# Performance work log

Hardware: AMD Instinct MI355X
Metric: run time of the kernel (lower is better)

The kernel has to match this reference:

```python
import jax, jax.numpy as jnp
import numpy as np

N_NODES = 50000

def _gcn_layer(x, src, dst, W, b, n_nodes):
    # x: [N, F_in]; src/dst: [E+N] (self-loops already appended)
    h = x @ W  # [N, F_out]
    deg = jax.ops.segment_sum(jnp.ones_like(dst, dtype=h.dtype), dst, num_segments=n_nodes)
    dinv = jnp.where(deg > 0, jax.lax.rsqrt(deg), 0.0)  # deg^{-1/2}
    norm = dinv[src] * dinv[dst]  # [E+N]
    msg = h[src] * norm[:, None]  # gather + scale
    out = jax.ops.segment_sum(msg, dst, num_segments=n_nodes)  # scatter-add
    return out + b

def setup_inputs() -> dict:
    key = jax.random.key(0)
    k1, k2, k3, k4 = jax.random.split(key, 4)
    d = 128
    E = 800000
    x = jax.random.normal(k1, (N_NODES, d), dtype=jnp.float32)
    edge_index = jax.random.randint(k2, (2, E), 0, N_NODES, dtype=jnp.int64)
    W1 = jax.random.normal(k3, (d, d), dtype=jnp.float32) / np.sqrt(d)
    b1 = jnp.zeros((d,), dtype=jnp.float32)
    W2 = jax.random.normal(k4, (d, d), dtype=jnp.float32) / np.sqrt(d)
    b2 = jnp.zeros((d,), dtype=jnp.float32)
    return {"x": x, "edge_index": edge_index, "W1": W1, "b1": b1, "W2": W2, "b2": b2}

def reference(x, edge_index, W1, b1, W2, b2):
    n = x.shape[0]
    loops = jnp.arange(n, dtype=edge_index.dtype)
    src = jnp.concatenate([edge_index[0], loops])  # add self-loops
    dst = jnp.concatenate([edge_index[1], loops])
    h = _gcn_layer(x, src, dst, W1, b1, n)
    h = jax.nn.relu(h)
    z = _gcn_layer(h, src, dst, W2, b2, n)
    return z
```

## Files before the change

### kernel.cpp

```cpp
#include <hip/hip_runtime.h>
#include <hip/hip_fp16.h>

#define NF 128
#define KC 64
#define NPART 4
#define NPMAX 12544

typedef _Float16 half8 __attribute__((ext_vector_type(8)));
typedef _Float16 half4v __attribute__((ext_vector_type(4)));
typedef float    floatx4 __attribute__((ext_vector_type(4)));

__global__ __launch_bounds__(512) void count2_k(
    const int* __restrict__ dst, unsigned short* __restrict__ pcnt,
    int E, int N, int Ec)
{
    __shared__ int lcnt[NPMAX];
    const int p = blockIdx.x & 3, c = blockIdx.x >> 2;
    const int Np = (N + 3) >> 2;
    const int lo = p * Np, hi = min(lo + Np, N);
    const int sz = hi - lo;
    for (int i = threadIdx.x; i < sz; i += 512) lcnt[i] = 0;
    __syncthreads();

    const int e0 = c * Ec, e1 = min(e0 + Ec, E);
    for (int e = e0 + (int)threadIdx.x * 4; e + 3 < e1; e += 512 * 4) {
        int4 d = *(const int4*)(dst + e);
        if (d.x >= lo && d.x < hi) atomicAdd(&lcnt[d.x - lo], 1);
        if (d.y >= lo && d.y < hi) atomicAdd(&lcnt[d.y - lo], 1);
        if (d.z >= lo && d.z < hi) atomicAdd(&lcnt[d.z - lo], 1);
        if (d.w >= lo && d.w < hi) atomicAdd(&lcnt[d.w - lo], 1);
    }
    int rem0 = e0 + ((e1 - e0) & ~3);
    for (int e = rem0 + (int)threadIdx.x; e < e1; e += 512) {
        int d = dst[e];
        if (d >= lo && d < hi) atomicAdd(&lcnt[d - lo], 1);
    }
    __syncthreads();
    for (int i = threadIdx.x; i < sz; i += 512)
        pcnt[(size_t)c * N + lo + i] = (unsigned short)lcnt[i];
}

__global__ __launch_bounds__(256) void pscan2_k(
    unsigned short* __restrict__ pcnt, float* __restrict__ dinv,
    int* __restrict__ rowptr, int* __restrict__ blocksum, int n, int N, int nb,
    const float* __restrict__ W1, const float* __restrict__ W2,
    __half* __restrict__ WT1, __half* __restrict__ WT2)
{
    if ((int)blockIdx.x >= nb) {
        int idx = ((int)blockIdx.x - nb) * 256 + threadIdx.x;
        const float* W = (idx < 16384) ? W1 : W2;
        __half* WT     = (idx < 16384) ? WT1 : WT2;
        int j = idx & 16383;
        int nn = j & 127, k = j >> 7;
        WT[nn * NF + k] = __float2half(W[k * NF + nn]);
        return;
    }
    __shared__ int sm[256];
    int tid = threadIdx.x;
    int bin = blockIdx.x * 256 + tid;
    int total = 0;
    if (bin < n) {
        #pragma unroll 4
        for (int c = 0; c < KC; c++) {
            size_t o = (size_t)c * N + bin;
            int v = pcnt[o];
            pcnt[o] = (unsigned short)total;
            total += v;
        }
        dinv[bin] = rsqrtf((float)total + 1.0f);
    }
    sm[tid] = total;
    __syncthreads();
    #pragma unroll
    for (int d = 1; d < 256; d <<= 1) {
        int t = (tid >= d) ? sm[tid - d] : 0;
        __syncthreads();
        sm[tid] += t;
        __syncthreads();
    }
    if (bin < n) rowptr[bin] = sm[tid] - total;
    if (tid == 255) blocksum[blockIdx.x] = sm[255];
}


template<bool F32IN>
__device__ __forceinline__ void gemm_body512(
    const void* __restrict__ Xv, const __half* __restrict__ WT,
    const float* __restrict__ dinv, __half* __restrict__ out, int M, int bid,
    __half (*wlds)[136])
{
    const int tid = threadIdx.x;
    {
        int r = tid >> 2;
        int c0 = (tid & 3) * 32;
        const half8* s = (const half8*)(WT + (size_t)r * NF + c0);
        half8* d = (half8*)&wlds[r][c0];
        #pragma unroll
        for (int j = 0; j < 4; j++) d[j] = s[j];
    }
    __syncthreads();

    const int wave = tid >> 6, lane = tid & 63;
    const int quad = lane >> 4, l15 = lane & 15;
    const int rowA = bid * 128 + wave * 16 + l15;
    const int rowc = (rowA < M) ? rowA : (M - 1);

    half8 afr[4];
    if (F32IN) {
        const float* X = (const float*)Xv;
        #pragma unroll
        for (int kc = 0; kc < 4; kc++) {
            const floatx4* p = (const floatx4*)(X + (size_t)rowc * NF + kc * 32 + quad * 8);
            floatx4 u = p[0], v = p[1];
            half8 a;
            a[0] = (_Float16)u[0]; a[1] = (_Float16)u[1];
            a[2] = (_Float16)u[2]; a[3] = (_Float16)u[3];
            a[4] = (_Float16)v[0]; a[5] = (_Float16)v[1];
            a[6] = (_Float16)v[2]; a[7] = (_Float16)v[3];
            afr[kc] = a;
        }
    } else {
        const __half* X = (const __half*)Xv;
        #pragma unroll
        for (int kc = 0; kc < 4; kc++)
            afr[kc] = *(const half8*)(X + (size_t)rowc * NF + kc * 32 + quad * 8);
    }

    floatx4 acc[8];
    #pragma unroll
    for (int ct = 0; ct < 8; ct++) { floatx4 z = {0.f, 0.f, 0.f, 0.f}; acc[ct] = z; }

    #pragma unroll
    for (int kc = 0; kc < 4; kc++) {
        #pragma unroll
        for (int ct = 0; ct < 8; ct++) {
            half8 b = *(const half8*)&wlds[ct * 16 + l15][kc * 32 + quad * 8];
            acc[ct] = __builtin_amdgcn_mfma_f32_16x16x32_f16(afr[kc], b, acc[ct], 0, 0, 0);
        }
    }

    const int orow0 = bid * 128 + wave * 16 + quad * 4;
    #pragma unroll
    for (int r = 0; r < 4; r++) {
        int orow = orow0 + r;
        if (orow < M) {
            float s = dinv[orow];
            #pragma unroll
            for (int ct = 0; ct < 8; ct++)
                out[(size_t)orow * NF + ct * 16 + l15] = __float2half(acc[ct][r] * s);
        }
    }
}

__global__ __launch_bounds__(512) void mid_k(
    const int* __restrict__ src, const int* __restrict__ dst,
    const int* __restrict__ rowptr, const unsigned short* __restrict__ coff,
    const int* __restrict__ blocksum, int* __restrict__ rowptr2,
    int* __restrict__ csr, int E, int N, int Ec, int nb,
    const float* __restrict__ X, const __half* __restrict__ WT,
    const float* __restrict__ dinv, __half* __restrict__ H, int GB2)
{
    __shared__ __align__(16) char smem[NPMAX * 4 + 1024];
    const int tid = threadIdx.x;
    if ((int)blockIdx.x < GB2) {
        gemm_body512<true>(X, WT, dinv, H, N, blockIdx.x, (__half(*)[136])smem);
        return;
    }
    int* lcur = (int*)smem;
    int* pref = (int*)(smem + NPMAX * 4);

    const int b = blockIdx.x - GB2;
    const int p = b & 3, c = b >> 2;
    const int Np = (N + 3) >> 2;
    const int lo = p * Np, hi = min(lo + Np, N);
    const int sz = hi - lo;

    int v = (tid < nb) ? blocksum[tid] : 0;
    if (tid < 256) pref[tid] = v;
    __syncthreads();
    #pragma unroll
    for (int d = 1; d < 256; d <<= 1) {
        int t = (tid < 256 && tid >= d) ? pref[tid - d] : 0;
        __syncthreads();
        if (tid < 256) pref[tid] += t;
        __syncthreads();
    }
    if (tid < 256) pref[tid] -= v;
    __syncthreads();

    for (int i = tid; i < sz; i += 512) {
        int bin = lo + i;
        int r = rowptr[bin] + pref[bin >> 8] + (int)coff[(size_t)c * N + bin];
        lcur[i] = r;
        if (c == 0) rowptr2[bin] = r;
    }
    if (c == 0 && p == 0 && tid == 0) rowptr2[N] = E;
    __syncthreads();

    const int e0 = c * Ec, e1 = min(e0 + Ec, E);
    for (int e = e0 + tid * 4; e + 3 < e1; e += 512 * 4) {
        int4 d = *(const int4*)(dst + e);
        int4 s = *(const int4*)(src + e);
        if (d.x >= lo && d.x < hi) csr[atomicAdd(&lcur[d.x - lo], 1)] = s.x;
        if (d.y >= lo && d.y < hi) csr[atomicAdd(&lcur[d.y - lo], 1)] = s.y;
        if (d.z >= lo && d.z < hi) csr[atomicAdd(&lcur[d.z - lo], 1)] = s.z;
        if (d.w >= lo && d.w < hi) csr[atomicAdd(&lcur[d.w - lo], 1)] = s.w;
    }
    int rem0 = e0 + ((e1 - e0) & ~3);
    for (int e = rem0 + tid; e < e1; e += 512) {
        int d = dst[e];
        if (d >= lo && d < hi) csr[atomicAdd(&lcur[d - lo], 1)] = src[e];
    }
}

template<bool F32IN>
__device__ __forceinline__ void gemm_body256(
    const void* __restrict__ Xv, const __half* __restrict__ WT,
    const float* __restrict__ dinv, __half* __restrict__ out, int M, int bid)
{
    __shared__ __half wlds[128][136];
    const int tid = threadIdx.x;
    {
        int r = tid >> 1;
        int c0 = (tid & 1) * 64;
        const half8* s = (const half8*)(WT + (size_t)r * NF + c0);
        half8* d = (half8*)&wlds[r][c0];
        #pragma unroll
        for (int j = 0; j < 8; j++) d[j] = s[j];
    }
    __syncthreads();

    const int wave = tid >> 6, lane = tid & 63;
    const int quad = lane >> 4, l15 = lane & 15;
    const int rowA = bid * 64 + wave * 16 + l15;
    const int rowc = (rowA < M) ? rowA : (M - 1);

    half8 afr[4];
    const __half* X = (const __half*)Xv;
    #pragma unroll
    for (int kc = 0; kc < 4; kc++)
        afr[kc] = *(const half8*)(X + (size_t)rowc * NF + kc * 32 + quad * 8);

    floatx4 acc[8];
    #pragma unroll
    for (int ct = 0; ct < 8; ct++) { floatx4 z = {0.f, 0.f, 0.f, 0.f}; acc[ct] = z; }

    #pragma unroll
    for (int kc = 0; kc < 4; kc++) {
        #pragma unroll
        for (int ct = 0; ct < 8; ct++) {
            half8 b = *(const half8*)&wlds[ct * 16 + l15][kc * 32 + quad * 8];
            acc[ct] = __builtin_amdgcn_mfma_f32_16x16x32_f16(afr[kc], b, acc[ct], 0, 0, 0);
        }
    }

    const int orow0 = bid * 64 + wave * 16 + quad * 4;
    #pragma unroll
    for (int r = 0; r < 4; r++) {
        int orow = orow0 + r;
        if (orow < M) {
            float s = dinv[orow];
            #pragma unroll
            for (int ct = 0; ct < 8; ct++)
                out[(size_t)orow * NF + ct * 16 + l15] = __float2half(acc[ct][r] * s);
        }
    }
}

__global__ __launch_bounds__(256) void gemm2_k(
    const __half* __restrict__ A, const __half* __restrict__ WT,
    const float* __restrict__ dinv, __half* __restrict__ H, int M)
{
    gemm_body256<false>(A, WT, dinv, H, M, blockIdx.x);
}


__global__ __launch_bounds__(256) void agg_k(
    const __half* __restrict__ hs, const int* __restrict__ rowptr,
    const int* __restrict__ csr, const float* __restrict__ dinv,
    const float* __restrict__ bias, __half* __restrict__ outh,
    float* __restrict__ outf, int n)
{
    int wave = threadIdx.x >> 6;
    int lane = threadIdx.x & 63;
    int node = blockIdx.x * 4 + wave;
    if (node >= n) return;
    const int eg = lane >> 5, fl = lane & 31;

    const half4v* hs4 = (const half4v*)hs;
    floatx4 acc = {0.f, 0.f, 0.f, 0.f};
    if (eg == 0) {
        half4v s = hs4[(size_t)node * 32 + fl];
        acc[0] = (float)s[0]; acc[1] = (float)s[1];
        acc[2] = (float)s[2]; acc[3] = (float)s[3];
    }

    int base = rowptr[node];
    int cnt  = rowptr[node + 1] - base;

    for (int off = 0; off < cnt; off += 64) {
        int m = min(64, cnt - off);
        int idx = 0;
        if (lane < m) idx = __builtin_nontemporal_load(&csr[base + off + lane]);
        for (int j = 0; j < m; j += 16) {
            int s[8];
            half4v v[8];
            #pragma unroll
            for (int t = 0; t < 8; t++)
                s[t] = __shfl(idx, min(j + 2 * t + eg, m - 1), 64);
            #pragma unroll
            for (int t = 0; t < 8; t++)
                v[t] = hs4[(size_t)s[t] * 32 + fl];
            #pragma unroll
            for (int t = 0; t < 8; t++) {
                if (j + 2 * t + eg < m) {
                    acc[0] += (float)v[t][0]; acc[1] += (float)v[t][1];
                    acc[2] += (float)v[t][2]; acc[3] += (float)v[t][3];
                }
            }
        }
    }

    #pragma unroll
    for (int k = 0; k < 4; k++) acc[k] += __shfl_xor(acc[k], 32, 64);

    if (eg == 0) {
        float dv = dinv[node];
        float o0 = dv * acc[0] + bias[fl * 4];
        float o1 = dv * acc[1] + bias[fl * 4 + 1];
        float o2 = dv * acc[2] + bias[fl * 4 + 2];
        float o3 = dv * acc[3] + bias[fl * 4 + 3];
        if (outh) {
            half4v h;
            h[0] = (_Float16)fmaxf(o0, 0.f); h[1] = (_Float16)fmaxf(o1, 0.f);
            h[2] = (_Float16)fmaxf(o2, 0.f); h[3] = (_Float16)fmaxf(o3, 0.f);
            *(half4v*)&outh[(size_t)node * NF + fl * 4] = h;
        } else {
            floatx4 w = {o0, o1, o2, o3};
            *(floatx4*)(outf + (size_t)node * NF + fl * 4) = w;
        }
    }
}


extern "C" void kernel_launch(void* const* d_in, const int* in_sizes, int n_in,
                              void* d_out, int out_size, void* d_ws, size_t ws_size,
                              hipStream_t stream) {
    const float* x  = (const float*)d_in[0];
    const int*   ei = (const int*)d_in[1];
    const float* W1 = (const float*)d_in[2];
    const float* b1 = (const float*)d_in[3];
    const float* W2 = (const float*)d_in[4];
    const float* b2 = (const float*)d_in[5];
    float* out = (float*)d_out;

    const int N = in_sizes[0] / NF;
    const int E = in_sizes[1] / 2;
    const int* src = ei;
    const int* dst = ei + E;

    char* ws = (char*)d_ws;
    size_t off = 0;
    auto alloc = [&](size_t bytes) {
        void* p = ws + off;
        off += bytes;
        off = (off + 63) & ~(size_t)63;
        return p;
    };
    unsigned short* pcnt = (unsigned short*)alloc((size_t)KC * N * 2);
    int*    rowptr  = (int*)alloc((size_t)(N + 1) * 4);
    int*    rowptr2 = (int*)alloc((size_t)(N + 1) * 4);
    int*    csr     = (int*)alloc((size_t)E * 4);
    float*  dinv    = (float*)alloc((size_t)N * 4);
    int*    bsum    = (int*)alloc((size_t)256 * 4);
    __half* WT1     = (__half*)alloc((size_t)NF * NF * 2);
    __half* WT2     = (__half*)alloc((size_t)NF * NF * 2);
    __half* H16     = (__half*)alloc((size_t)N * NF * 2);
    __half* A16     = (__half*)alloc((size_t)N * NF * 2);

    int nb  = (N + 255) / 256;
    int Ec  = (((E + KC - 1) / KC) + 3) & ~3;
    int GB2 = (N + 127) / 128;
    int gb  = (N + 63) / 64;
    int ab  = (N + 3) / 4;

    count2_k<<<KC * NPART, 512, 0, stream>>>(dst, pcnt, E, N, Ec);
    pscan2_k<<<nb + 128, 256, 0, stream>>>(pcnt, dinv, rowptr, bsum, N, N, nb,
                                           W1, W2, WT1, WT2);
    mid_k<<<GB2 + KC * NPART, 512, 0, stream>>>(src, dst, rowptr, pcnt, bsum,
                                                rowptr2, csr, E, N, Ec, nb,
                                                x, WT1, dinv, H16, GB2);
    agg_k<<<ab, 256, 0, stream>>>(H16, rowptr2, csr, dinv, b1, A16, nullptr, N);
    gemm2_k<<<gb, 256, 0, stream>>>(A16, WT2, dinv, H16, N);
    agg_k<<<ab, 256, 0, stream>>>(H16, rowptr2, csr, dinv, b2, nullptr, out, N);
}
```

Baseline: 210.3 us.

## Fuse layer-1 aggregation with layer-2 GEMM and shrink per-chunk counts to bytes

Replaces the separate layer-1 aggregation kernel and layer-2 GEMM with one kernel. Each block gathers 16 node rows into LDS, applies bias and ReLU, then multiplies by W2 with MFMA. This drops the A16 intermediate's round trip through global memory and one launch. The gather inner loop is unrolled to 16 loads in flight, and the per-chunk count/offset array is narrowed from 16-bit to 8-bit to halve its traffic. In exchange, every small block reloads the full 32KB W2 tile into LDS, which also limits occupancy. Byte offsets overflow for any node with in-degree above 255.

```diff
diff --git a/kernel.cpp b/kernel.cpp
--- a/kernel.cpp
+++ b/kernel.cpp
@@ -6,12 +6,12 @@
 #define NPART 4
 #define NPMAX 12544
 
-typedef _Float16 half8 __attribute__((ext_vector_type(8)));
+typedef _Float16 half8  __attribute__((ext_vector_type(8)));
 typedef _Float16 half4v __attribute__((ext_vector_type(4)));
 typedef float    floatx4 __attribute__((ext_vector_type(4)));
 
 __global__ __launch_bounds__(512) void count2_k(
-    const int* __restrict__ dst, unsigned short* __restrict__ pcnt,
+    const int* __restrict__ dst, unsigned char* __restrict__ pcnt,
     int E, int N, int Ec)
 {
     __shared__ int lcnt[NPMAX];
@@ -37,11 +37,11 @@
     }
     __syncthreads();
     for (int i = threadIdx.x; i < sz; i += 512)
-        pcnt[(size_t)c * N + lo + i] = (unsigned short)lcnt[i];
+        pcnt[(size_t)c * N + lo + i] = (unsigned char)lcnt[i];
 }
 
 __global__ __launch_bounds__(256) void pscan2_k(
-    unsigned short* __restrict__ pcnt, float* __restrict__ dinv,
+    unsigned char* __restrict__ pcnt, float* __restrict__ dinv,
     int* __restrict__ rowptr, int* __restrict__ blocksum, int n, int N, int nb,
     const float* __restrict__ W1, const float* __restrict__ W2,
     __half* __restrict__ WT1, __half* __restrict__ WT2)
@@ -64,7 +64,7 @@
         for (int c = 0; c < KC; c++) {
             size_t o = (size_t)c * N + bin;
             int v = pcnt[o];
-            pcnt[o] = (unsigned short)total;
+            pcnt[o] = (unsigned char)total;
             total += v;
         }
         dinv[bin] = rsqrtf((float)total + 1.0f);
@@ -81,7 +81,6 @@
     if (bin < n) rowptr[bin] = sm[tid] - total;
     if (tid == 255) blocksum[blockIdx.x] = sm[255];
 }
-
 
 template<bool F32IN>
 __device__ __forceinline__ void gemm_body512(
@@ -154,7 +153,7 @@
 
 __global__ __launch_bounds__(512) void mid_k(
     const int* __restrict__ src, const int* __restrict__ dst,
-    const int* __restrict__ rowptr, const unsigned short* __restrict__ coff,
+    const int* __restrict__ rowptr, const unsigned char* __restrict__ coff,
     const int* __restrict__ blocksum, int* __restrict__ rowptr2,
     int* __restrict__ csr, int E, int N, int Ec, int nb,
     const float* __restrict__ X, const __half* __restrict__ WT,
@@ -213,73 +212,117 @@
     }
 }
 
-template<bool F32IN>
-__device__ __forceinline__ void gemm_body256(
-    const void* __restrict__ Xv, const __half* __restrict__ WT,
-    const float* __restrict__ dinv, __half* __restrict__ out, int M, int bid)
+__device__ __forceinline__ floatx4 gather_acc(
+    const half4v* __restrict__ hs4, const int* __restrict__ csr,
+    int base, int cnt, int node, int eg, int fl, int lane)
+{
+    floatx4 acc = {0.f, 0.f, 0.f, 0.f};
+    if (eg == 0) {
+        half4v s = hs4[(size_t)node * 32 + fl];
+        acc[0] = (float)s[0]; acc[1] = (float)s[1];
+        acc[2] = (float)s[2]; acc[3] = (float)s[3];
+    }
+    for (int off = 0; off < cnt; off += 64) {
+        int m = min(64, cnt - off);
+        int idx = 0;
+        if (lane < m) idx = __builtin_nontemporal_load(&csr[base + off + lane]);
+        for (int j = 0; j < m; j += 32) {
+            int s[16];
+            half4v v[16];
+            #pragma unroll
+            for (int t = 0; t < 16; t++)
+                s[t] = __shfl(idx, min(j + 2 * t + eg, m - 1), 64);
+            #pragma unroll
+            for (int t = 0; t < 16; t++)
+                v[t] = hs4[(size_t)s[t] * 32 + fl];
+            #pragma unroll
+            for (int t = 0; t < 16; t++) {
+                if (j + 2 * t + eg < m) {
+                    acc[0] += (float)v[t][0]; acc[1] += (float)v[t][1];
+                    acc[2] += (float)v[t][2]; acc[3] += (float)v[t][3];
+                }
+            }
+        }
+    }
+    #pragma unroll
+    for (int k = 0; k < 4; k++) acc[k] += __shfl_xor(acc[k], 32, 64);
+    return acc;
+}
+
+__global__ __launch_bounds__(256) void aggemm_k(
+    const __half* __restrict__ hs, const int* __restrict__ rowptr,
+    const int* __restrict__ csr, const float* __restrict__ dinv,
+    const float* __restrict__ bias, const __half* __restrict__ WT2,
+    __half* __restrict__ H2, int n)
 {
     __shared__ __half wlds[128][136];
+    __shared__ __half arow[16][136];
     const int tid = threadIdx.x;
     {
-        int r = tid >> 1;
-        int c0 = (tid & 1) * 64;
-        const half8* s = (const half8*)(WT + (size_t)r * NF + c0);
+        int r = tid >> 1, c0 = (tid & 1) * 64;
+        const half8* s = (const half8*)(WT2 + (size_t)r * NF + c0);
         half8* d = (half8*)&wlds[r][c0];
         #pragma unroll
         for (int j = 0; j < 8; j++) d[j] = s[j];
     }
-    __syncthreads();
 
     const int wave = tid >> 6, lane = tid & 63;
+    const int eg = lane >> 5, fl = lane & 31;
+    const half4v* hs4 = (const half4v*)hs;
+
+    #pragma unroll
+    for (int u = 0; u < 4; u++) {
+        int node = blockIdx.x * 16 + wave * 4 + u;
+        if (node < n) {
+            int base = rowptr[node];
+            int cnt  = rowptr[node + 1] - base;
+            floatx4 acc = gather_acc(hs4, csr, base, cnt, node, eg, fl, lane);
+            if (eg == 0) {
+                float dv = dinv[node];
+                half4v h;
+                h[0] = (_Float16)fmaxf(dv * acc[0] + bias[fl * 4 + 0], 0.f);
+                h[1] = (_Float16)fmaxf(dv * acc[1] + bias[fl * 4 + 1], 0.f);
+                h[2] = (_Float16)fmaxf(dv * acc[2] + bias[fl * 4 + 2], 0.f);
+                h[3] = (_Float16)fmaxf(dv * acc[3] + bias[fl * 4 + 3], 0.f);
+                *(half4v*)&arow[wave * 4 + u][fl * 4] = h;
+            }
+        } else if (eg == 0) {
+            half4v z = {(_Float16)0.f, (_Float16)0.f, (_Float16)0.f, (_Float16)0.f};
+            *(half4v*)&arow[wave * 4 + u][fl * 4] = z;
+        }
+    }
+    __syncthreads();
+
     const int quad = lane >> 4, l15 = lane & 15;
-    const int rowA = bid * 64 + wave * 16 + l15;
-    const int rowc = (rowA < M) ? rowA : (M - 1);
-
     half8 afr[4];
-    const __half* X = (const __half*)Xv;
     #pragma unroll
     for (int kc = 0; kc < 4; kc++)
-        afr[kc] = *(const half8*)(X + (size_t)rowc * NF + kc * 32 + quad * 8);
-
-    floatx4 acc[8];
-    #pragma unroll
-    for (int ct = 0; ct < 8; ct++) { floatx4 z = {0.f, 0.f, 0.f, 0.f}; acc[ct] = z; }
-
+        afr[kc] = *(const half8*)&arow[l15][kc * 32 + quad * 8];
+
+    floatx4 acc0 = {0.f, 0.f, 0.f, 0.f}, acc1 = {0.f, 0.f, 0.f, 0.f};
+    const int ct0 = wave * 2, ct1 = wave * 2 + 1;
     #pragma unroll
     for (int kc = 0; kc < 4; kc++) {
-        #pragma unroll
-        for (int ct = 0; ct < 8; ct++) {
-            half8 b = *(const half8*)&wlds[ct * 16 + l15][kc * 32 + quad * 8];
-            acc[ct] = __builtin_amdgcn_mfma_f32_16x16x32_f16(afr[kc], b, acc[ct], 0, 0, 0);
-        }
-    }
-
-    const int orow0 = bid * 64 + wave * 16 + quad * 4;
+        half8 b0 = *(const half8*)&wlds[ct0 * 16 + l15][kc * 32 + quad * 8];
+        half8 b1 = *(const half8*)&wlds[ct1 * 16 + l15][kc * 32 + quad * 8];
+        acc0 = __builtin_amdgcn_mfma_f32_16x16x32_f16(afr[kc], b0, acc0, 0, 0, 0);
+        acc1 = __builtin_amdgcn_mfma_f32_16x16x32_f16(afr[kc], b1, acc1, 0, 0, 0);
+    }
     #pragma unroll
     for (int r = 0; r < 4; r++) {
-        int orow = orow0 + r;
-        if (orow < M) {
-            float s = dinv[orow];
-            #pragma unroll
-            for (int ct = 0; ct < 8; ct++)
-                out[(size_t)orow * NF + ct * 16 + l15] = __float2half(acc[ct][r] * s);
-        }
-    }
-}
-
-__global__ __launch_bounds__(256) void gemm2_k(
-    const __half* __restrict__ A, const __half* __restrict__ WT,
-    const float* __restrict__ dinv, __half* __restrict__ H, int M)
-{
-    gemm_body256<false>(A, WT, dinv, H, M, blockIdx.x);
-}
-
-
-__global__ __launch_bounds__(256) void agg_k(
+        int node = blockIdx.x * 16 + quad * 4 + r;
+        if (node < n) {
+            float s = dinv[node];
+            H2[(size_t)node * NF + ct0 * 16 + l15] = __float2half(acc0[r] * s);
+            H2[(size_t)node * NF + ct1 * 16 + l15] = __float2half(acc1[r] * s);
+        }
+    }
+}
+
+__global__ __launch_bounds__(256) void agg2_k(
     const __half* __restrict__ hs, const int* __restrict__ rowptr,
     const int* __restrict__ csr, const float* __restrict__ dinv,
-    const float* __restrict__ bias, __half* __restrict__ outh,
-    float* __restrict__ outf, int n)
+    const float* __restrict__ bias, float* __restrict__ outf, int n)
 {
     int wave = threadIdx.x >> 6;
     int lane = threadIdx.x & 63;
@@ -287,58 +330,18 @@
     if (node >= n) return;
     const int eg = lane >> 5, fl = lane & 31;
 
-    const half4v* hs4 = (const half4v*)hs;
-    floatx4 acc = {0.f, 0.f, 0.f, 0.f};
-    if (eg == 0) {
-        half4v s = hs4[(size_t)node * 32 + fl];
-        acc[0] = (float)s[0]; acc[1] = (float)s[1];
-        acc[2] = (float)s[2]; acc[3] = (float)s[3];
-    }
-
     int base = rowptr[node];
     int cnt  = rowptr[node + 1] - base;
-
-    for (int off = 0; off < cnt; off += 64) {
-        int m = min(64, cnt - off);
-        int idx = 0;
-        if (lane < m) idx = __builtin_nontemporal_load(&csr[base + off + lane]);
-        for (int j = 0; j < m; j += 16) {
-            int s[8];
-            half4v v[8];
-            #pragma unroll
-            for (int t = 0; t < 8; t++)
-                s[t] = __shfl(idx, min(j + 2 * t + eg, m - 1), 64);
-            #pragma unroll
-            for (int t = 0; t < 8; t++)
-                v[t] = hs4[(size_t)s[t] * 32 + fl];
-            #pragma unroll
-            for (int t = 0; t < 8; t++) {
-                if (j + 2 * t + eg < m) {
-                    acc[0] += (float)v[t][0]; acc[1] += (float)v[t][1];
-                    acc[2] += (float)v[t][2]; acc[3] += (float)v[t][3];
-                }
-            }
-        }
-    }
-
-    #pragma unroll
-    for (int k = 0; k < 4; k++) acc[k] += __shfl_xor(acc[k], 32, 64);
+    floatx4 acc = gather_acc((const half4v*)hs, csr, base, cnt, node, eg, fl, lane);
 
     if (eg == 0) {
         float dv = dinv[node];
-        float o0 = dv * acc[0] + bias[fl * 4];
-        float o1 = dv * acc[1] + bias[fl * 4 + 1];
-        float o2 = dv * acc[2] + bias[fl * 4 + 2];
-        float o3 = dv * acc[3] + bias[fl * 4 + 3];
-        if (outh) {
-            half4v h;
-            h[0] = (_Float16)fmaxf(o0, 0.f); h[1] = (_Float16)fmaxf(o1, 0.f);
-            h[2] = (_Float16)fmaxf(o2, 0.f); h[3] = (_Float16)fmaxf(o3, 0.f);
-            *(half4v*)&outh[(size_t)node * NF + fl * 4] = h;
-        } else {
-            floatx4 w = {o0, o1, o2, o3};
-            *(floatx4*)(outf + (size_t)node * NF + fl * 4) = w;
-        }
+        floatx4 w;
+        w[0] = dv * acc[0] + bias[fl * 4 + 0];
+        w[1] = dv * acc[1] + bias[fl * 4 + 1];
+        w[2] = dv * acc[2] + bias[fl * 4 + 2];
+        w[3] = dv * acc[3] + bias[fl * 4 + 3];
+        *(floatx4*)(outf + (size_t)node * NF + fl * 4) = w;
     }
 }
 
@@ -367,7 +370,7 @@
         off = (off + 63) & ~(size_t)63;
         return p;
     };
-    unsigned short* pcnt = (unsigned short*)alloc((size_t)KC * N * 2);
+    unsigned char* pcnt = (unsigned char*)alloc((size_t)KC * N);
     int*    rowptr  = (int*)alloc((size_t)(N + 1) * 4);
     int*    rowptr2 = (int*)alloc((size_t)(N + 1) * 4);
     int*    csr     = (int*)alloc((size_t)E * 4);
@@ -376,12 +379,12 @@
     __half* WT1     = (__half*)alloc((size_t)NF * NF * 2);
     __half* WT2     = (__half*)alloc((size_t)NF * NF * 2);
     __half* H16     = (__half*)alloc((size_t)N * NF * 2);
-    __half* A16     = (__half*)alloc((size_t)N * NF * 2);
+    __half* H2      = (__half*)alloc((size_t)N * NF * 2);
 
     int nb  = (N + 255) / 256;
     int Ec  = (((E + KC - 1) / KC) + 3) & ~3;
     int GB2 = (N + 127) / 128;
-    int gb  = (N + 63) / 64;
+    int ag1 = (N + 15) / 16;
     int ab  = (N + 3) / 4;
 
     count2_k<<<KC * NPART, 512, 0, stream>>>(dst, pcnt, E, N, Ec);
@@ -390,7 +393,6 @@
     mid_k<<<GB2 + KC * NPART, 512, 0, stream>>>(src, dst, rowptr, pcnt, bsum,
                                                 rowptr2, csr, E, N, Ec, nb,
                                                 x, WT1, dinv, H16, GB2);
-    agg_k<<<ab, 256, 0, stream>>>(H16, rowptr2, csr, dinv, b1, A16, nullptr, N);
-    gemm2_k<<<gb, 256, 0, stream>>>(A16, WT2, dinv, H16, N);
-    agg_k<<<ab, 256, 0, stream>>>(H16, rowptr2, csr, dinv, b2, nullptr, out, N);
-}
+    aggemm_k<<<ag1, 256, 0, stream>>>(H16, rowptr2, csr, dinv, b1, WT2, H2, N);
+    agg2_k<<<ab, 256, 0, stream>>>(H2, rowptr2, csr, dinv, b2, out, N);
+}
```

After: 223.3 us. 6.2% more time.
